# Kernel tuning notes

Measured on AMD Instinct MI355X. Metric: run time of the kernel, lower is better.

Reference implementation:

```python
import jax, jax.numpy as jnp
import numpy as np

ALPHA = 0.2
BN_EPS = 1e-5
NEG = -9e15


def make_quaternion_mul(kernel):
    # kernel: [in/4, out]; split columns into quaternion components
    dim = kernel.shape[1] // 4
    r, i, j, k = jnp.split(kernel, 4, axis=1)
    r2 = jnp.concatenate([r, -i, -j, -k], axis=0)
    i2 = jnp.concatenate([i, r, -k, j], axis=0)
    j2 = jnp.concatenate([j, k, r, -i], axis=0)
    k2 = jnp.concatenate([k, -j, i, r], axis=0)
    return jnp.concatenate([r2, i2, j2, k2], axis=1)  # [in, out]


def setup_inputs() -> dict:
    key = jax.random.key(0)
    k1, k2, k3, k4 = jax.random.split(key, 4)
    N, IN, OUT = 8192, 512, 128
    inp = jax.random.normal(k1, (N, IN), dtype=jnp.float32)
    adj = jax.random.randint(k2, (N, N), 0, 2, dtype=jnp.int32)
    # xavier-like init for params
    W = jax.random.normal(k3, (IN // 4, OUT), dtype=jnp.float32) * (1.0 / np.sqrt(IN // 4))
    a = jax.random.normal(k4, (2 * OUT, 1), dtype=jnp.float32) * (1.0 / np.sqrt(2 * OUT))
    bn_gamma = jnp.ones((OUT,), dtype=jnp.float32)
    bn_beta = jnp.zeros((OUT,), dtype=jnp.float32)
    return {"input": inp, "adj": adj, "W": W, "a": a, "bn_gamma": bn_gamma, "bn_beta": bn_beta}


def reference(input, adj, W, a, bn_gamma, bn_beta):
    out_features = W.shape[1]
    hamilton = make_quaternion_mul(W)           # [in, out]
    h = input @ hamilton                        # [N, out]
    # a_input[i,j] = concat(h_i, h_j); a_input @ a decomposes as
    # (h @ a1)_i + (h @ a2)_j with a1 = a[:out], a2 = a[out:]
    a1 = a[:out_features, 0]                    # [out]
    a2 = a[out_features:, 0]                    # [out]
    s1 = h @ a1                                 # [N]
    s2 = h @ a2                                 # [N]
    e = s1[:, None] + s2[None, :]               # [N, N]
    e = jnp.where(e > 0, e, ALPHA * e)          # leaky_relu
    attention = jnp.where(adj > 0, e, NEG)
    attention = jax.nn.softmax(attention, axis=1)
    # dropout is identity in inference
    h_prime = attention @ h                     # [N, out]
    # BatchNorm1d (training-mode batch statistics, biased variance)
    mean = jnp.mean(h_prime, axis=0)
    var = jnp.var(h_prime, axis=0)
    h_prime = (h_prime - mean) / jnp.sqrt(var + BN_EPS) * bn_gamma + bn_beta
    # concat=True -> ELU
    return jax.nn.elu(h_prime)
```

## Files before the change

### kernel.cpp

```cpp
#include <hip/hip_runtime.h>
#include <hip/hip_bf16.h>
#include <math.h>

#define N_NODES 8192
#define IN_F    512
#define OUT_F   128
#define LRELU_A 0.2f
#define EPS_BN  1e-5f
#define MSH     40.0f
#define NSPLIT  16
#define JSPAN   (N_NODES / NSPLIT)
#define TILE_I  128
#define CH      128
#define HSTR    520

typedef unsigned short u16;
typedef unsigned int   u32;
typedef __attribute__((ext_vector_type(8))) short  short8;
typedef __attribute__((ext_vector_type(4))) float  floatx4;

__device__ __forceinline__ u16 f2bf_rtn(float x) {
    u32 u = __float_as_uint(x);
    return (u16)((u + 0x7fffu + ((u >> 16) & 1u)) >> 16);
}

__global__ __launch_bounds__(256) void k_h(const float* __restrict__ inp, const float* __restrict__ W,
                                           const float* __restrict__ a,
                                           u16* __restrict__ hT, float* __restrict__ s1, float* __restrict__ s2,
                                           float* __restrict__ cs, float* __restrict__ cq) {
    __shared__ float s1b[16], s2b[16];
    const int t = threadIdx.x;
    if (t < 16) { s1b[t] = 0.f; s2b[t] = 0.f; }
    if (blockIdx.x == 0 && t < OUT_F) { cs[t] = 0.f; cq[t] = 0.f; }
    __syncthreads();
    const int rg = t >> 4, cg = t & 15;
    const int r = blockIdx.x * 16 + rg;
    const int b = cg >> 2, cc0 = (cg & 3) * 8;
    const u32 NEGMASK = 0x284Eu;
    float acc[8];
#pragma unroll
    for (int q = 0; q < 8; q++) acc[q] = 0.f;
    const float* row = inp + (size_t)r * IN_F;
    for (int k8 = 0; k8 < IN_F; k8 += 8) {
        const int p = k8 >> 7;
        const float sg = (NEGMASK >> (b * 4 + p)) & 1u ? -1.f : 1.f;
        const float* wbase = W + (b ^ p) * 32 + cc0;
        float4 x0 = *(const float4*)(row + k8);
        float4 x1 = *(const float4*)(row + k8 + 4);
        float xv[8] = {x0.x, x0.y, x0.z, x0.w, x1.x, x1.y, x1.z, x1.w};
#pragma unroll
        for (int dk = 0; dk < 8; dk++) {
            const int q = (k8 + dk) & 127;
            const float* wp = wbase + q * 128;
            float4 w0 = *(const float4*)wp;
            float4 w1 = *(const float4*)(wp + 4);
            const float av = xv[dk] * sg;
            acc[0] += av * w0.x; acc[1] += av * w0.y; acc[2] += av * w0.z; acc[3] += av * w0.w;
            acc[4] += av * w1.x; acc[5] += av * w1.y; acc[6] += av * w1.z; acc[7] += av * w1.w;
        }
    }
    float s1p = 0.f, s2p = 0.f;
#pragma unroll
    for (int q = 0; q < 8; q++) {
        const int c = (cg << 3) + q;
        hT[(size_t)c * N_NODES + r] = f2bf_rtn(acc[q]);
        s1p += acc[q] * a[c];
        s2p += acc[q] * a[OUT_F + c];
    }
    atomicAdd(&s1b[rg], s1p);
    atomicAdd(&s2b[rg], s2p);
    __syncthreads();
    if (t < 16) { s1[blockIdx.x * 16 + t] = s1b[t]; s2[blockIdx.x * 16 + t] = s2b[t]; }
}

__global__ __launch_bounds__(512, 2) void k_att(const int* __restrict__ adj, const u16* __restrict__ hT,
                                                const float* __restrict__ s1, const float* __restrict__ s2,
                                                float* __restrict__ Opart, float* __restrict__ Lpart) {
    __shared__ u16 hs[128 * HSTR];
    __shared__ float s2s[JSPAN];
    const int t = threadIdx.x;
    const int lane = t & 63, wid = t >> 6;
    const int quad = lane >> 4, n = lane & 15;
    const int i0 = blockIdx.x * TILE_I;
    const int jbase = blockIdx.y * JSPAN;
    const int i_lane = i0 + wid * 16 + n;
    const float s1v = s1[i_lane];

    if (t < 128) *(float4*)&s2s[t * 4] = *(const float4*)&s2[jbase + t * 4];
    {
        const int cr = t >> 2, off = (t & 3) * 128;
        const u16* src = hT + (size_t)cr * N_NODES + jbase + off;
        u16* dst = &hs[cr * HSTR + off];
#pragma unroll
        for (int v = 0; v < 16; v++)
            *(uint4*)(dst + v * 8) = *(const uint4*)(src + v * 8);
    }

    floatx4 acc[8];
#pragma unroll
    for (int ct = 0; ct < 8; ct++) acc[ct] = (floatx4){0.f, 0.f, 0.f, 0.f};
    float Lacc = 0.f;

    const int* adjp = adj + (size_t)i_lane * N_NODES + jbase;
    uint4 P[8];
#pragma unroll
    for (int ks = 0; ks < 4; ks++) {
        P[2 * ks]     = *(const uint4*)(adjp + ks * 32 + quad * 8);
        P[2 * ks + 1] = *(const uint4*)(adjp + ks * 32 + quad * 8 + 4);
    }
    __syncthreads();

#pragma unroll
    for (int k = 0; k < JSPAN / CH; k++) {
        uint4 C[8];
#pragma unroll
        for (int v = 0; v < 8; v++) C[v] = P[v];
        if (k + 1 < JSPAN / CH) {
            const int* ap = adjp + (k + 1) * CH;
#pragma unroll
            for (int ks = 0; ks < 4; ks++) {
                P[2 * ks]     = *(const uint4*)(ap + ks * 32 + quad * 8);
                P[2 * ks + 1] = *(const uint4*)(ap + ks * 32 + quad * 8 + 4);
            }
        }
        short8 fa[4];
#pragma unroll
        for (int ks = 0; ks < 4; ks++) {
            const int jl = k * CH + ks * 32 + quad * 8;
            float4 sa = *(const float4*)&s2s[jl];
            float4 sb = *(const float4*)&s2s[jl + 4];
            const float sv[8] = {sa.x, sa.y, sa.z, sa.w, sb.x, sb.y, sb.z, sb.w};
            const u32 am[8] = {C[2*ks].x, C[2*ks].y, C[2*ks].z, C[2*ks].w,
                               C[2*ks+1].x, C[2*ks+1].y, C[2*ks+1].z, C[2*ks+1].w};
#pragma unroll
            for (int jj = 0; jj < 8; jj++) {
                float sc = s1v + sv[jj];
                sc = fmaxf(sc, LRELU_A * sc);
                float w = ((int)am[jj] > 0) ? __expf(sc - MSH) : 0.f;
                Lacc += w;
                fa[ks][jj] = (short)f2bf_rtn(w);
            }
        }
#pragma unroll
        for (int ks = 0; ks < 4; ks++) {
#pragma unroll
            for (int ct = 0; ct < 8; ct++) {
                short8 fb = *(const short8*)&hs[(ct * 16 + n) * HSTR + k * CH + ks * 32 + quad * 8];
                acc[ct] = __builtin_amdgcn_mfma_f32_16x16x32_bf16(fa[ks], fb, acc[ct], 0, 0, 0);
            }
        }
    }

    Lacc += __shfl_xor(Lacc, 16, 64);
    Lacc += __shfl_xor(Lacc, 32, 64);
    if (lane < 16)
        Lpart[(size_t)blockIdx.y * N_NODES + i_lane] = Lacc;

    const size_t obase = (size_t)blockIdx.y * N_NODES * OUT_F;
#pragma unroll
    for (int ct = 0; ct < 8; ct++) {
#pragma unroll
        for (int r = 0; r < 4; r++) {
            const int i = i0 + wid * 16 + quad * 4 + r;
            Opart[obase + (size_t)i * OUT_F + ct * 16 + n] = acc[ct][r];
        }
    }
}

__global__ __launch_bounds__(256) void k_comb(const float* __restrict__ Opart, const float* __restrict__ Lpart,
                                              float* __restrict__ hp, float* __restrict__ cs, float* __restrict__ cq) {
    const int t = threadIdx.x;
    const int c = t & 127, half = t >> 7;
    const int ibase = blockIdx.x * 16;
    float sv = 0.f, sq = 0.f;
    for (int k = 0; k < 8; k++) {
        const int i = ibase + half + (k << 1);
        float o = 0.f, L = 0.f;
#pragma unroll
        for (int s = 0; s < NSPLIT; s++) {
            o += Opart[((size_t)s * N_NODES + i) * OUT_F + c];
            L += Lpart[(size_t)s * N_NODES + i];
        }
        float v = L > 0.f ? o / L : 0.f;
        hp[(size_t)i * OUT_F + c] = v;
        sv += v; sq += v * v;
    }
    __shared__ float red[256];
    red[t] = sv; __syncthreads();
    if (half == 0) atomicAdd(&cs[c], sv + red[t + 128]);
    __syncthreads(); red[t] = sq; __syncthreads();
    if (half == 0) atomicAdd(&cq[c], sq + red[t + 128]);
}

__global__ __launch_bounds__(256) void k_bn(const float* __restrict__ hp, const float* __restrict__ cs,
                                            const float* __restrict__ cq, const float* __restrict__ gamma,
                                            const float* __restrict__ beta, float* __restrict__ out) {
    const int idx = blockIdx.x * 256 + threadIdx.x;
    const int c = idx & 127;
    const float mean = cs[c] * (1.f / N_NODES);
    const float var  = cq[c] * (1.f / N_NODES) - mean * mean;
    float x = (hp[idx] - mean) * rsqrtf(var + EPS_BN) * gamma[c] + beta[c];
    x = x > 0.f ? x : expm1f(x);
    out[idx] = x;
}

extern "C" void kernel_launch(void* const* d_in, const int* in_sizes, int n_in,
                              void* d_out, int out_size, void* d_ws, size_t ws_size,
                              hipStream_t stream) {
    (void)in_sizes; (void)n_in; (void)out_size; (void)ws_size;
    const float* inp   = (const float*)d_in[0];
    const int*   adj   = (const int*)d_in[1];
    const float* W     = (const float*)d_in[2];
    const float* a     = (const float*)d_in[3];
    const float* gamma = (const float*)d_in[4];
    const float* beta  = (const float*)d_in[5];
    float* out = (float*)d_out;

    char* wsb = (char*)d_ws;
    u16*   hT  = (u16*)wsb;    wsb += (size_t)OUT_F * N_NODES * 2;
    float* s1  = (float*)wsb;  wsb += N_NODES * 4;
    float* s2  = (float*)wsb;  wsb += N_NODES * 4;
    float* Op  = (float*)wsb;  wsb += (size_t)NSPLIT * N_NODES * OUT_F * 4;
    float* Lp  = (float*)wsb;  wsb += (size_t)NSPLIT * N_NODES * 4;
    float* hp  = (float*)wsb;  wsb += (size_t)N_NODES * OUT_F * 4;
    float* cs  = (float*)wsb;  wsb += OUT_F * 4;
    float* cq  = (float*)wsb;  wsb += OUT_F * 4;

    hipLaunchKernelGGL(k_h,    dim3(512), dim3(256), 0, stream, inp, W, a, hT, s1, s2, cs, cq);
    hipLaunchKernelGGL(k_att,  dim3(64, NSPLIT), dim3(512), 0, stream, adj, hT, s1, s2, Op, Lp);
    hipLaunchKernelGGL(k_comb, dim3(512), dim3(256), 0, stream, Op, Lp, hp, cs, cq);
    hipLaunchKernelGGL(k_bn,   dim3(4096), dim3(256), 0, stream, hp, cs, cq, gamma, beta, out);
}
```

Measured before the change: 530.6 us.

## Preload adjacency tile with coalesced loads and ballot-pack into shared bitmask

The attention kernel now loads each wave's 16 rows of the adjacency slice with fully coalesced row-contiguous loads up front, packs them into bitmasks via wavefront ballots, and stores them in shared memory. The main loop then reads mask bits from registers instead of issuing strided per-lane adjacency loads inside the loop. Separately, the projection kernel stages W in shared memory. This gives better-coalesced adjacency traffic and fewer registers for prefetch buffers, at the cost of a serialized upfront load phase that no longer overlaps with MFMA work.

```diff
diff --git a/kernel.cpp b/kernel.cpp
--- a/kernel.cpp
+++ b/kernel.cpp
@@ -13,9 +13,11 @@
 #define TILE_I  128
 #define CH      128
 #define HSTR    520
+#define MWORDS  16
 
 typedef unsigned short u16;
 typedef unsigned int   u32;
+typedef unsigned long long u64;
 typedef __attribute__((ext_vector_type(8))) short  short8;
 typedef __attribute__((ext_vector_type(4))) float  floatx4;
 
@@ -28,10 +30,16 @@
                                            const float* __restrict__ a,
                                            u16* __restrict__ hT, float* __restrict__ s1, float* __restrict__ s2,
                                            float* __restrict__ cs, float* __restrict__ cq) {
+    __shared__ float Wl[128 * 128];
     __shared__ float s1b[16], s2b[16];
     const int t = threadIdx.x;
     if (t < 16) { s1b[t] = 0.f; s2b[t] = 0.f; }
     if (blockIdx.x == 0 && t < OUT_F) { cs[t] = 0.f; cq[t] = 0.f; }
+#pragma unroll
+    for (int i = 0; i < 16; i++) {
+        const int idx = t * 4 + i * 1024;
+        *(float4*)&Wl[idx] = *(const float4*)&W[idx];
+    }
     __syncthreads();
     const int rg = t >> 4, cg = t & 15;
     const int r = blockIdx.x * 16 + rg;
@@ -43,8 +51,8 @@
     const float* row = inp + (size_t)r * IN_F;
     for (int k8 = 0; k8 < IN_F; k8 += 8) {
         const int p = k8 >> 7;
-        const float sg = (NEGMASK >> (b * 4 + p)) & 1u ? -1.f : 1.f;
-        const float* wbase = W + (b ^ p) * 32 + cc0;
+        const float sg = ((NEGMASK >> (b * 4 + p)) & 1u) ? -1.f : 1.f;
+        const float* wbase = Wl + (b ^ p) * 32 + cc0;
         float4 x0 = *(const float4*)(row + k8);
         float4 x1 = *(const float4*)(row + k8 + 4);
         float xv[8] = {x0.x, x0.y, x0.z, x0.w, x1.x, x1.y, x1.z, x1.w};
@@ -73,11 +81,29 @@
     if (t < 16) { s1[blockIdx.x * 16 + t] = s1b[t]; s2[blockIdx.x * 16 + t] = s2b[t]; }
 }
 
+__device__ __forceinline__ void pack_row(const uint4& h0, const uint4& h1, u32* mp, int lane) {
+    u64 c0 = __ballot((int)h0.x > 0);
+    u64 c1 = __ballot((int)h0.y > 0);
+    u64 c2 = __ballot((int)h0.z > 0);
+    u64 c3 = __ballot((int)h0.w > 0);
+    u64 d0 = __ballot((int)h1.x > 0);
+    u64 d1 = __ballot((int)h1.y > 0);
+    u64 d2 = __ballot((int)h1.z > 0);
+    u64 d3 = __ballot((int)h1.w > 0);
+    if (lane == 0) {
+        *(uint4*)(mp)      = make_uint4((u32)c0, (u32)(c0 >> 32), (u32)c1, (u32)(c1 >> 32));
+        *(uint4*)(mp + 4)  = make_uint4((u32)c2, (u32)(c2 >> 32), (u32)c3, (u32)(c3 >> 32));
+        *(uint4*)(mp + 8)  = make_uint4((u32)d0, (u32)(d0 >> 32), (u32)d1, (u32)(d1 >> 32));
+        *(uint4*)(mp + 12) = make_uint4((u32)d2, (u32)(d2 >> 32), (u32)d3, (u32)(d3 >> 32));
+    }
+}
+
 __global__ __launch_bounds__(512, 2) void k_att(const int* __restrict__ adj, const u16* __restrict__ hT,
                                                 const float* __restrict__ s1, const float* __restrict__ s2,
                                                 float* __restrict__ Opart, float* __restrict__ Lpart) {
     __shared__ u16 hs[128 * HSTR];
     __shared__ float s2s[JSPAN];
+    __shared__ u32 mk[8 * 16 * MWORDS];
     const int t = threadIdx.x;
     const int lane = t & 63, wid = t >> 6;
     const int quad = lane >> 4, n = lane & 15;
@@ -96,33 +122,57 @@
             *(uint4*)(dst + v * 8) = *(const uint4*)(src + v * 8);
     }
 
+    {
+        const int* abase = adj + (size_t)(i0 + wid * 16) * N_NODES + jbase + lane * 4;
+        u32* mwp = &mk[(wid * 16) * MWORDS];
+        uint4 P0[8], P1[8];
+#pragma unroll
+        for (int rr = 0; rr < 4; rr++) {
+            P0[2 * rr]     = *(const uint4*)(abase + (size_t)rr * N_NODES);
+            P0[2 * rr + 1] = *(const uint4*)(abase + (size_t)rr * N_NODES + 256);
+        }
+#pragma unroll
+        for (int rr = 0; rr < 4; rr++) {
+            P1[2 * rr]     = *(const uint4*)(abase + (size_t)(4 + rr) * N_NODES);
+            P1[2 * rr + 1] = *(const uint4*)(abase + (size_t)(4 + rr) * N_NODES + 256);
+        }
+#pragma unroll
+        for (int rr = 0; rr < 4; rr++) pack_row(P0[2 * rr], P0[2 * rr + 1], mwp + rr * MWORDS, lane);
+#pragma unroll
+        for (int rr = 0; rr < 4; rr++) {
+            P0[2 * rr]     = *(const uint4*)(abase + (size_t)(8 + rr) * N_NODES);
+            P0[2 * rr + 1] = *(const uint4*)(abase + (size_t)(8 + rr) * N_NODES + 256);
+        }
+#pragma unroll
+        for (int rr = 0; rr < 4; rr++) pack_row(P1[2 * rr], P1[2 * rr + 1], mwp + (4 + rr) * MWORDS, lane);
+#pragma unroll
+        for (int rr = 0; rr < 4; rr++) {
+            P1[2 * rr]     = *(const uint4*)(abase + (size_t)(12 + rr) * N_NODES);
+            P1[2 * rr + 1] = *(const uint4*)(abase + (size_t)(12 + rr) * N_NODES + 256);
+        }
+#pragma unroll
+        for (int rr = 0; rr < 4; rr++) pack_row(P0[2 * rr], P0[2 * rr + 1], mwp + (8 + rr) * MWORDS, lane);
+#pragma unroll
+        for (int rr = 0; rr < 4; rr++) pack_row(P1[2 * rr], P1[2 * rr + 1], mwp + (12 + rr) * MWORDS, lane);
+    }
+    __syncthreads();
+
+    u32 m32[16];
+    {
+        const u32* mp = &mk[(wid * 16 + n) * MWORDS];
+        *(uint4*)&m32[0]  = *(const uint4*)(mp);
+        *(uint4*)&m32[4]  = *(const uint4*)(mp + 4);
+        *(uint4*)&m32[8]  = *(const uint4*)(mp + 8);
+        *(uint4*)&m32[12] = *(const uint4*)(mp + 12);
+    }
+
     floatx4 acc[8];
 #pragma unroll
     for (int ct = 0; ct < 8; ct++) acc[ct] = (floatx4){0.f, 0.f, 0.f, 0.f};
     float Lacc = 0.f;
 
-    const int* adjp = adj + (size_t)i_lane * N_NODES + jbase;
-    uint4 P[8];
-#pragma unroll
-    for (int ks = 0; ks < 4; ks++) {
-        P[2 * ks]     = *(const uint4*)(adjp + ks * 32 + quad * 8);
-        P[2 * ks + 1] = *(const uint4*)(adjp + ks * 32 + quad * 8 + 4);
-    }
-    __syncthreads();
-
 #pragma unroll
     for (int k = 0; k < JSPAN / CH; k++) {
-        uint4 C[8];
-#pragma unroll
-        for (int v = 0; v < 8; v++) C[v] = P[v];
-        if (k + 1 < JSPAN / CH) {
-            const int* ap = adjp + (k + 1) * CH;
-#pragma unroll
-            for (int ks = 0; ks < 4; ks++) {
-                P[2 * ks]     = *(const uint4*)(ap + ks * 32 + quad * 8);
-                P[2 * ks + 1] = *(const uint4*)(ap + ks * 32 + quad * 8 + 4);
-            }
-        }
         short8 fa[4];
 #pragma unroll
         for (int ks = 0; ks < 4; ks++) {
@@ -130,13 +180,14 @@
             float4 sa = *(const float4*)&s2s[jl];
             float4 sb = *(const float4*)&s2s[jl + 4];
             const float sv[8] = {sa.x, sa.y, sa.z, sa.w, sb.x, sb.y, sb.z, sb.w};
-            const u32 am[8] = {C[2*ks].x, C[2*ks].y, C[2*ks].z, C[2*ks].w,
-                               C[2*ks+1].x, C[2*ks+1].y, C[2*ks+1].z, C[2*ks+1].w};
+            const int bit32 = ks * 8 + quad * 2;
 #pragma unroll
             for (int jj = 0; jj < 8; jj++) {
+                const u32 word = m32[(k >> 1) * 8 + (jj & 3) * 2 + (k & 1)];
+                const u32 mbit = (word >> (bit32 + (jj >> 2))) & 1u;
                 float sc = s1v + sv[jj];
                 sc = fmaxf(sc, LRELU_A * sc);
-                float w = ((int)am[jj] > 0) ? __expf(sc - MSH) : 0.f;
+                float w = mbit ? __expf(sc - MSH) : 0.f;
                 Lacc += w;
                 fa[ks][jj] = (short)f2bf_rtn(w);
             }
```

After: 513.5 us. 3.2% less time.

## Pack adjacency into bitmask and restructure attention kernel to stream h from L2

Applied to the files above, without the earlier changes.

A new pre-pass kernel turns the int32 adjacency matrix into a bitmask using wave ballots. The attention kernel then reads one bit per entry instead of one int per entry. The attention kernel also drops its large LDS copy of h and reads h fragments directly from global/L2. It uses smaller 32-row tiles, with two waves splitting the output channels, and cuts the j-split from 16 to 4, which shrinks the partial-output buffers that the combine kernel has to re-read. Separately, the h projection kernel stages W in shared memory. The costs are an extra full pass over adj and heavier L2 traffic for h fragments without LDS reuse.

```diff
diff --git a/kernel.cpp b/kernel.cpp
--- a/kernel.cpp
+++ b/kernel.cpp
@@ -8,30 +8,58 @@
 #define LRELU_A 0.2f
 #define EPS_BN  1e-5f
 #define MSH     40.0f
-#define NSPLIT  16
+#define NSPLIT  4
 #define JSPAN   (N_NODES / NSPLIT)
-#define TILE_I  128
-#define CH      128
-#define HSTR    520
+#define TILE_I  32
 
 typedef unsigned short u16;
 typedef unsigned int   u32;
+typedef unsigned long long u64;
 typedef __attribute__((ext_vector_type(8))) short  short8;
 typedef __attribute__((ext_vector_type(4))) float  floatx4;
 
 __device__ __forceinline__ u16 f2bf_rtn(float x) {
     u32 u = __float_as_uint(x);
     return (u16)((u + 0x7fffu + ((u >> 16) & 1u)) >> 16);
+}
+
+__global__ __launch_bounds__(256) void k_pack(const int* __restrict__ adj, u32* __restrict__ mask) {
+    const int t = threadIdx.x;
+    const int lane = t & 63, wid = t >> 6;
+    const int row = blockIdx.x * 4 + wid;
+    const int* ap = adj + (size_t)row * N_NODES + lane * 4;
+    u32* mp = mask + (size_t)row * 256;
+    uint4 cur = *(const uint4*)(ap);
+#pragma unroll 4
+    for (int g = 0; g < 32; ++g) {
+        uint4 nxt = cur;
+        if (g + 1 < 32) nxt = *(const uint4*)(ap + (g + 1) * 256);
+        u64 b0 = __ballot((int)cur.x > 0);
+        u64 b1 = __ballot((int)cur.y > 0);
+        u64 b2 = __ballot((int)cur.z > 0);
+        u64 b3 = __ballot((int)cur.w > 0);
+        if (lane < 4) {
+            u64 v = (lane == 0) ? b0 : (lane == 1) ? b1 : (lane == 2) ? b2 : b3;
+            *(u64*)(mp + g * 8 + lane * 2) = v;
+        }
+        cur = nxt;
+    }
 }
 
 __global__ __launch_bounds__(256) void k_h(const float* __restrict__ inp, const float* __restrict__ W,
                                            const float* __restrict__ a,
                                            u16* __restrict__ hT, float* __restrict__ s1, float* __restrict__ s2,
                                            float* __restrict__ cs, float* __restrict__ cq) {
+    __shared__ float Wl[128 * 128];
     __shared__ float s1b[16], s2b[16];
     const int t = threadIdx.x;
     if (t < 16) { s1b[t] = 0.f; s2b[t] = 0.f; }
     if (blockIdx.x == 0 && t < OUT_F) { cs[t] = 0.f; cq[t] = 0.f; }
+#pragma unroll
+    for (int i = 0; i < 16; i++) {
+        const int idx = t * 4 + i * 1024;
+        *(float4*)&Wl[idx] = *(const float4*)&W[idx];
+    }
     __syncthreads();
     const int rg = t >> 4, cg = t & 15;
     const int r = blockIdx.x * 16 + rg;
@@ -43,8 +71,8 @@
     const float* row = inp + (size_t)r * IN_F;
     for (int k8 = 0; k8 < IN_F; k8 += 8) {
         const int p = k8 >> 7;
-        const float sg = (NEGMASK >> (b * 4 + p)) & 1u ? -1.f : 1.f;
-        const float* wbase = W + (b ^ p) * 32 + cc0;
+        const float sg = ((NEGMASK >> (b * 4 + p)) & 1u) ? -1.f : 1.f;
+        const float* wbase = Wl + (b ^ p) * 32 + cc0;
         float4 x0 = *(const float4*)(row + k8);
         float4 x1 = *(const float4*)(row + k8 + 4);
         float xv[8] = {x0.x, x0.y, x0.z, x0.w, x1.x, x1.y, x1.z, x1.w};
@@ -73,96 +101,104 @@
     if (t < 16) { s1[blockIdx.x * 16 + t] = s1b[t]; s2[blockIdx.x * 16 + t] = s2b[t]; }
 }
 
-__global__ __launch_bounds__(512, 2) void k_att(const int* __restrict__ adj, const u16* __restrict__ hT,
+__global__ __launch_bounds__(256, 3) void k_att(const u32* __restrict__ mask, const u16* __restrict__ hT,
                                                 const float* __restrict__ s1, const float* __restrict__ s2,
                                                 float* __restrict__ Opart, float* __restrict__ Lpart) {
-    __shared__ u16 hs[128 * HSTR];
     __shared__ float s2s[JSPAN];
     const int t = threadIdx.x;
     const int lane = t & 63, wid = t >> 6;
     const int quad = lane >> 4, n = lane & 15;
+    const int ib = wid >> 1, ch = wid & 1;
     const int i0 = blockIdx.x * TILE_I;
     const int jbase = blockIdx.y * JSPAN;
-    const int i_lane = i0 + wid * 16 + n;
+    const int i_lane = i0 + ib * 16 + n;
     const float s1v = s1[i_lane];
 
-    if (t < 128) *(float4*)&s2s[t * 4] = *(const float4*)&s2[jbase + t * 4];
     {
-        const int cr = t >> 2, off = (t & 3) * 128;
-        const u16* src = hT + (size_t)cr * N_NODES + jbase + off;
-        u16* dst = &hs[cr * HSTR + off];
-#pragma unroll
-        for (int v = 0; v < 16; v++)
-            *(uint4*)(dst + v * 8) = *(const uint4*)(src + v * 8);
-    }
-
-    floatx4 acc[8];
-#pragma unroll
-    for (int ct = 0; ct < 8; ct++) acc[ct] = (floatx4){0.f, 0.f, 0.f, 0.f};
+        const int o = t * 8;
+        *(float4*)&s2s[o]     = *(const float4*)&s2[jbase + o];
+        *(float4*)&s2s[o + 4] = *(const float4*)&s2[jbase + o + 4];
+    }
+
+    const u32* mrow = mask + (size_t)i_lane * 256 + (jbase >> 5);
+    uint4 mgA = *(const uint4*)(mrow);
+    uint4 mgB = *(const uint4*)(mrow + 4);
+
+    floatx4 acc[4];
+#pragma unroll
+    for (int ct = 0; ct < 4; ct++) acc[ct] = (floatx4){0.f, 0.f, 0.f, 0.f};
     float Lacc = 0.f;
-
-    const int* adjp = adj + (size_t)i_lane * N_NODES + jbase;
-    uint4 P[8];
-#pragma unroll
-    for (int ks = 0; ks < 4; ks++) {
-        P[2 * ks]     = *(const uint4*)(adjp + ks * 32 + quad * 8);
-        P[2 * ks + 1] = *(const uint4*)(adjp + ks * 32 + quad * 8 + 4);
-    }
+    const int quad2 = quad * 2;
+
     __syncthreads();
 
-#pragma unroll
-    for (int k = 0; k < JSPAN / CH; k++) {
-        uint4 C[8];
-#pragma unroll
-        for (int v = 0; v < 8; v++) C[v] = P[v];
-        if (k + 1 < JSPAN / CH) {
-            const int* ap = adjp + (k + 1) * CH;
-#pragma unroll
-            for (int ks = 0; ks < 4; ks++) {
-                P[2 * ks]     = *(const uint4*)(ap + ks * 32 + quad * 8);
-                P[2 * ks + 1] = *(const uint4*)(ap + ks * 32 + quad * 8 + 4);
+#pragma unroll 2
+    for (int g = 0; g < 8; ++g) {
+        uint4 mgA_n = mgA, mgB_n = mgB;
+        if (g + 1 < 8) {
+            mgA_n = *(const uint4*)(mrow + (g + 1) * 8);
+            mgB_n = *(const uint4*)(mrow + (g + 1) * 8 + 4);
+        }
+        const u32 mg[8] = {mgA.x, mgA.y, mgA.z, mgA.w, mgB.x, mgB.y, mgB.z, mgB.w};
+#pragma unroll
+        for (int p = 0; p < 2; ++p) {
+            const int jc = g * 2 + p;
+            short8 fb[16];
+#pragma unroll
+            for (int ct = 0; ct < 4; ++ct) {
+                const u16* hr = hT + (size_t)((ch * 4 + ct) * 16 + n) * N_NODES
+                              + jbase + jc * 128 + quad * 8;
+#pragma unroll
+                for (int ks = 0; ks < 4; ++ks)
+                    fb[ct * 4 + ks] = *(const short8*)(hr + ks * 32);
             }
-        }
-        short8 fa[4];
-#pragma unroll
-        for (int ks = 0; ks < 4; ks++) {
-            const int jl = k * CH + ks * 32 + quad * 8;
-            float4 sa = *(const float4*)&s2s[jl];
-            float4 sb = *(const float4*)&s2s[jl + 4];
-            const float sv[8] = {sa.x, sa.y, sa.z, sa.w, sb.x, sb.y, sb.z, sb.w};
-            const u32 am[8] = {C[2*ks].x, C[2*ks].y, C[2*ks].z, C[2*ks].w,
-                               C[2*ks+1].x, C[2*ks+1].y, C[2*ks+1].z, C[2*ks+1].w};
-#pragma unroll
-            for (int jj = 0; jj < 8; jj++) {
-                float sc = s1v + sv[jj];
-                sc = fmaxf(sc, LRELU_A * sc);
-                float w = ((int)am[jj] > 0) ? __expf(sc - MSH) : 0.f;
-                Lacc += w;
-                fa[ks][jj] = (short)f2bf_rtn(w);
+            short8 fa[4];
+#pragma unroll
+            for (int ks = 0; ks < 4; ++ks) {
+                const int jl = jc * 128 + ks * 32 + quad * 8;
+                float4 sa = *(const float4*)&s2s[jl];
+                float4 sb = *(const float4*)&s2s[jl + 4];
+                const float sv[8] = {sa.x, sa.y, sa.z, sa.w, sb.x, sb.y, sb.z, sb.w};
+                union { u32 u[4]; short8 s; } cv;
+#pragma unroll
+                for (int jh = 0; jh < 4; ++jh) {
+                    float w2[2];
+#pragma unroll
+                    for (int e = 0; e < 2; ++e) {
+                        const int jj = jh * 2 + e;
+                        const u32 word = mg[(jj & 3) * 2 + p];
+                        const u32 mbit = (word >> (ks * 8 + quad2 + (jj >> 2))) & 1u;
+                        float sc = s1v + sv[jj];
+                        sc = fmaxf(sc, LRELU_A * sc);
+                        float w = mbit ? __expf(sc - MSH) : 0.f;
+                        Lacc += w;
+                        w2[e] = w;
+                    }
+                    cv.u[jh] = (u32)f2bf_rtn(w2[0]) | ((u32)f2bf_rtn(w2[1]) << 16);
+                }
+                fa[ks] = cv.s;
             }
-        }
-#pragma unroll
-        for (int ks = 0; ks < 4; ks++) {
-#pragma unroll
-            for (int ct = 0; ct < 8; ct++) {
-                short8 fb = *(const short8*)&hs[(ct * 16 + n) * HSTR + k * CH + ks * 32 + quad * 8];
-                acc[ct] = __builtin_amdgcn_mfma_f32_16x16x32_bf16(fa[ks], fb, acc[ct], 0, 0, 0);
-            }
-        }
+#pragma unroll
+            for (int ks = 0; ks < 4; ++ks)
+#pragma unroll
+                for (int ct = 0; ct < 4; ++ct)
+                    acc[ct] = __builtin_amdgcn_mfma_f32_16x16x32_bf16(fa[ks], fb[ct * 4 + ks], acc[ct], 0, 0, 0);
+        }
+        mgA = mgA_n; mgB = mgB_n;
     }
 
     Lacc += __shfl_xor(Lacc, 16, 64);
     Lacc += __shfl_xor(Lacc, 32, 64);
-    if (lane < 16)
+    if (ch == 0 && lane < 16)
         Lpart[(size_t)blockIdx.y * N_NODES + i_lane] = Lacc;
 
     const size_t obase = (size_t)blockIdx.y * N_NODES * OUT_F;
 #pragma unroll
-    for (int ct = 0; ct < 8; ct++) {
-#pragma unroll
-        for (int r = 0; r < 4; r++) {
-            const int i = i0 + wid * 16 + quad * 4 + r;
-            Opart[obase + (size_t)i * OUT_F + ct * 16 + n] = acc[ct][r];
+    for (int ct = 0; ct < 4; ++ct) {
+#pragma unroll
+        for (int r = 0; r < 4; ++r) {
+            const int i = i0 + ib * 16 + quad * 4 + r;
+            Opart[obase + (size_t)i * OUT_F + (ch * 4 + ct) * 16 + n] = acc[ct][r];
         }
     }
 }
@@ -217,17 +253,19 @@
     float* out = (float*)d_out;
 
     char* wsb = (char*)d_ws;
-    u16*   hT  = (u16*)wsb;    wsb += (size_t)OUT_F * N_NODES * 2;
-    float* s1  = (float*)wsb;  wsb += N_NODES * 4;
-    float* s2  = (float*)wsb;  wsb += N_NODES * 4;
-    float* Op  = (float*)wsb;  wsb += (size_t)NSPLIT * N_NODES * OUT_F * 4;
-    float* Lp  = (float*)wsb;  wsb += (size_t)NSPLIT * N_NODES * 4;
-    float* hp  = (float*)wsb;  wsb += (size_t)N_NODES * OUT_F * 4;
-    float* cs  = (float*)wsb;  wsb += OUT_F * 4;
-    float* cq  = (float*)wsb;  wsb += OUT_F * 4;
-
+    u16*   hT   = (u16*)wsb;   wsb += (size_t)OUT_F * N_NODES * 2;
+    float* s1   = (float*)wsb; wsb += N_NODES * 4;
+    float* s2   = (float*)wsb; wsb += N_NODES * 4;
+    u32*   mask = (u32*)wsb;   wsb += (size_t)N_NODES * 256 * 4;
+    float* Op   = (float*)wsb; wsb += (size_t)NSPLIT * N_NODES * OUT_F * 4;
+    float* Lp   = (float*)wsb; wsb += (size_t)NSPLIT * N_NODES * 4;
+    float* hp   = (float*)wsb; wsb += (size_t)N_NODES * OUT_F * 4;
+    float* cs   = (float*)wsb; wsb += OUT_F * 4;
+    float* cq   = (float*)wsb; wsb += OUT_F * 4;
+
+    hipLaunchKernelGGL(k_pack, dim3(2048), dim3(256), 0, stream, adj, mask);
     hipLaunchKernelGGL(k_h,    dim3(512), dim3(256), 0, stream, inp, W, a, hT, s1, s2, cs, cq);
-    hipLaunchKernelGGL(k_att,  dim3(64, NSPLIT), dim3(512), 0, stream, adj, hT, s1, s2, Op, Lp);
+    hipLaunchKernelGGL(k_att,  dim3(256, NSPLIT), dim3(256), 0, stream, mask, hT, s1, s2, Op, Lp);
     hipLaunchKernelGGL(k_comb, dim3(512), dim3(256), 0, stream, Op, Lp, hp, cs, cq);
     hipLaunchKernelGGL(k_bn,   dim3(4096), dim3(256), 0, stream, hp, cs, cq, gamma, beta, out);
 }
```

New measurement: 551.1 us. 1.04x slower.
